# Optimization experiments

Hardware: AMD Instinct MI355X
Metric: run time of the kernel (lower is better)

The kernel has to match this reference:

```python
import jax, jax.numpy as jnp
import numpy as np

NEG_INF = -1.0e9
LEAKY_SLOPE = 0.2


def setup_inputs() -> dict:
    key = jax.random.key(0)
    ks = jax.random.split(key, 8)
    B, H, N, D = 4, 8, 256, 64
    query = jax.random.normal(ks[0], (B, H, N, D), dtype=jnp.float32)
    k_ = jax.random.normal(ks[1], (B, H, N, D), dtype=jnp.float32)
    value = jax.random.normal(ks[2], (B, H, N, D), dtype=jnp.float32)
    mask = jax.random.randint(ks[3], (B, 1, N, N), 0, 2, dtype=jnp.int32)
    # nn.Linear(d_k*2, d_k): weight (D, 2D), bias (D,)
    lim_h = 1.0 / np.sqrt(2 * D)
    W_h = jax.random.uniform(ks[4], (D, 2 * D), minval=-lim_h, maxval=lim_h, dtype=jnp.float32)
    b_h = jax.random.uniform(ks[5], (D,), minval=-lim_h, maxval=lim_h, dtype=jnp.float32)
    # nn.Linear(d_k, 1): weight (1, D), bias (1,)
    lim_o = 1.0 / np.sqrt(D)
    W_o = jax.random.uniform(ks[6], (1, D), minval=-lim_o, maxval=lim_o, dtype=jnp.float32)
    b_o = jax.random.uniform(ks[7], (1,), minval=-lim_o, maxval=lim_o, dtype=jnp.float32)
    return {"query": query, "key": k_, "value": value, "mask": mask,
            "W_h": W_h, "b_h": b_h, "W_o": W_o, "b_o": b_o}


def reference(query, key, value, mask, W_h, b_h, W_o, b_o):
    # W_h acts on concat([q, k]); decompose into two projections (same math):
    # W_h @ [q; k] = q @ W_q^T + k @ W_k^T
    D = query.shape[-1]
    Wq, Wk = W_h[:, :D], W_h[:, D:]
    q_proj = jnp.einsum('bhnd,ed->bhne', query, Wq)  # (B,H,N,D)
    k_proj = jnp.einsum('bhmd,ed->bhme', key, Wk)    # (B,H,N,D)
    # pairwise hidden: (B,H,N,N,D)
    hidden = q_proj[:, :, :, None, :] + k_proj[:, :, None, :, :] + b_h
    hidden = jax.nn.leaky_relu(hidden, negative_slope=LEAKY_SLOPE)
    scores = jnp.einsum('bhnme,e->bhnm', hidden, W_o[0]) + b_o[0]  # (B,H,N,N)
    scores = jnp.where(mask == 0, NEG_INF, scores)
    p_attn = jax.nn.softmax(scores, axis=-1)
    out = jnp.einsum('bhnm,bhmd->bhnd', p_attn, value)
    return out, p_attn
```

## Files before the change

### kernel.cpp

```cpp
#include <hip/hip_runtime.h>

typedef float v2f __attribute__((ext_vector_type(2)));
typedef _Float16 h8 __attribute__((ext_vector_type(8)));

constexpr int B = 4, H = 8, N = 256, D = 64;
constexpr int QBLK = 8;
constexpr int PATTN_OFF = B * H * N * D;
constexpr int NROWS = B * H * N;


__global__ __launch_bounds__(256, 2) void proj_kernel(
    const float* __restrict__ q, const float* __restrict__ k,
    const float* __restrict__ W_h, const float* __restrict__ b_h,
    const float* __restrict__ W_o, const float* __restrict__ b_o,
    float* __restrict__ qp, _Float16* __restrict__ kpbh,
    float* __restrict__ cq6, float* __restrict__ ck6, float* __restrict__ w4)
{
    __shared__ float WT[128 * 65];
    int t = threadIdx.x;
    int lane = t & 63;
    int wid = __builtin_amdgcn_readfirstlane(t >> 6);
    int bid = blockIdx.x;
    int work = (bid & 7) * 64 + (bid >> 3);

    #pragma unroll
    for (int i = 0; i < 8; ++i) {
        int fidx = (t + i * 256) * 4;
        float4 w = *reinterpret_cast<const float4*>(W_h + fidx);
        int e = fidx >> 7, d = fidx & 127;
        WT[(d + 0) * 65 + e] = w.x;
        WT[(d + 1) * 65 + e] = w.y;
        WT[(d + 2) * 65 + e] = w.z;
        WT[(d + 3) * 65 + e] = w.w;
    }
    if (bid == 0 && t < 64) w4[t] = 0.4f * W_o[t];
    __syncthreads();

    int rbase = work * 16 + wid * 4;
    float accq[4] = {}, acck[4] = {};
    #pragma unroll
    for (int d0 = 0; d0 < 64; d0 += 16) {
        float wq[16], wk[16];
        #pragma unroll
        for (int d = 0; d < 16; ++d) {
            wq[d] = WT[(d0 + d) * 65 + lane];
            wk[d] = WT[(64 + d0 + d) * 65 + lane];
        }
        #pragma unroll
        for (int j = 0; j < 4; ++j) {
            const float* qrow = q + (rbase + j) * 64 + d0;
            const float* krow = k + (rbase + j) * 64 + d0;
            #pragma unroll
            for (int d = 0; d < 16; ++d) {
                accq[j] = fmaf(qrow[d], wq[d], accq[j]);
                acck[j] = fmaf(krow[d], wk[d], acck[j]);
            }
        }
    }
    float bh_e = b_h[lane];
    float wo = W_o[lane];
    float bo = b_o[0];
    #pragma unroll
    for (int j = 0; j < 4; ++j) {
        float aq = accq[j];
        float ak = acck[j] + bh_e;
        qp[(rbase + j) * 64 + lane] = aq;
        kpbh[(rbase + j) * 64 + lane] = (_Float16)ak;
        float sq = wo * aq, sk = wo * ak;
        #pragma unroll
        for (int off = 32; off > 0; off >>= 1) {
            sq += __shfl_xor(sq, off, 64);
            sk += __shfl_xor(sk, off, 64);
        }
        if (lane == 0) {
            cq6[rbase + j] = 0.6f * sq + bo;
            ck6[rbase + j] = 0.6f * sk;
        }
    }
}

__global__ __launch_bounds__(512, 2) void attn_kernel(
    const float* __restrict__ qp, const _Float16* __restrict__ kpbh,
    const float* __restrict__ V, const int* __restrict__ mask,
    const float* __restrict__ cq6, const float* __restrict__ ck6,
    const float* __restrict__ w4g,
    float* __restrict__ out)
{
    __shared__ float sc[4096];
    __shared__ _Float16 pf[2048];
    __shared__ float red_s[8][4];

    int t = threadIdx.x;
    int lane = t & 63;
    int wid = __builtin_amdgcn_readfirstlane(t >> 6);
    int h = wid >> 2;
    int m = t & 255;
    int bid = blockIdx.x;
    int work = (bid & 7) * 128 + (bid >> 3);
    int bh = work >> 5;
    int nb = work & 31;
    int b = bh >> 3;
    int n0 = nb * QBLK;
    int kvbase = bh * N * 64;

    const h8* kph = reinterpret_cast<const h8*>(kpbh + kvbase + m * 64 + h * 32);
    h8 kh0 = kph[0], kh1 = kph[1], kh2 = kph[2], kh3 = kph[3];

    float mf[4];
    #pragma unroll
    for (int i = 0; i < 4; ++i)
        mf[i] = (mask[(b * N + n0 + h * 4 + i) * N + m] != 0) ? 1.0f : 0.0f;

    float ckt = (h == 0) ? ck6[bh * N + m] : 0.f;

    v2f sp2[8];
    const float* cq = cq6 + bh * N + n0;
    #pragma unroll
    for (int r = 0; r < 8; ++r) {
        float init = (h == 0) ? (cq[r] + ckt) : 0.f;
        sp2[r] = (v2f){init, 0.f};
    }

    const v2f* qr2 = reinterpret_cast<const v2f*>(qp + (bh * N + n0) * 64 + h * 32);
    const v2f* w42 = reinterpret_cast<const v2f*>(w4g + h * 32);
    #pragma unroll
    for (int chunk = 0; chunk < 4; ++chunk) {
        h8 kc = (chunk == 0) ? kh0 : (chunk == 1) ? kh1 : (chunk == 2) ? kh2 : kh3;
        #pragma unroll
        for (int p = 0; p < 4; ++p) {
            v2f w2 = w42[chunk * 4 + p];
            v2f k2 = (v2f){(float)kc[2 * p], (float)kc[2 * p + 1]};
            #pragma unroll
            for (int r = 0; r < 8; ++r) {
                v2f x = qr2[r * 32 + chunk * 4 + p] + k2;
                v2f ax = __builtin_elementwise_max(x, -x);
                sp2[r] = __builtin_elementwise_fma(w2, ax, sp2[r]);
            }
        }
    }
    #pragma unroll
    for (int r = 0; r < 8; ++r)
        sc[h * 2048 + r * 256 + m] = sp2[r].x + sp2[r].y;

    const float* Vp = V + kvbase + wid * 32 * 64 + lane;
    float vpre[8];
    #pragma unroll
    for (int g = 0; g < 8; ++g) vpre[g] = Vp[g * 64];
    __syncthreads();

    float p8[4];
    #pragma unroll
    for (int i = 0; i < 4; ++i) {
        int rr = h * 4 + i;
        float s = sc[rr * 256 + m] + sc[2048 + rr * 256 + m];
        float p = __expf(s) * mf[i];
        p8[i] = p;
        float l = p;
        #pragma unroll
        for (int off = 32; off > 0; off >>= 1) l += __shfl_xor(l, off, 64);
        if (lane == 0) red_s[wid][i] = l;
    }
    __syncthreads();

    #pragma unroll
    for (int i = 0; i < 4; ++i) {
        int rr = h * 4 + i;
        float gs = red_s[h*4+0][i] + red_s[h*4+1][i] + red_s[h*4+2][i] + red_s[h*4+3][i];
        float pn = p8[i] * __frcp_rn(gs);
        pf[rr * 256 + m] = (_Float16)pn;
        out[PATTN_OFF + (bh * N + n0 + rr) * N + m] = pn;
    }
    __syncthreads();

    float acc[8] = {};
    {
        #pragma unroll
        for (int r = 0; r < 8; ++r) {
            h8 ph = *reinterpret_cast<const h8*>(&pf[r * 256 + wid * 32]);
            #pragma unroll
            for (int g = 0; g < 8; ++g)
                acc[r] = fmaf((float)ph[g], vpre[g], acc[r]);
        }
    }
    #pragma unroll
    for (int j = 8; j < 32; j += 8) {
        float vv[8];
        #pragma unroll
        for (int g = 0; g < 8; ++g) vv[g] = Vp[(j + g) * 64];
        #pragma unroll
        for (int r = 0; r < 8; ++r) {
            h8 ph = *reinterpret_cast<const h8*>(&pf[r * 256 + wid * 32 + j]);
            #pragma unroll
            for (int g = 0; g < 8; ++g)
                acc[r] = fmaf((float)ph[g], vv[g], acc[r]);
        }
    }
    __syncthreads();

    #pragma unroll
    for (int r = 0; r < 8; ++r)
        sc[wid * 512 + r * 64 + lane] = acc[r];
    __syncthreads();

    float o = 0.f;
    #pragma unroll
    for (int mc = 0; mc < 8; ++mc)
        o += sc[mc * 512 + wid * 64 + lane];
    out[(bh * N + n0 + wid) * 64 + lane] = o;
}

extern "C" void kernel_launch(void* const* d_in, const int* in_sizes, int n_in,
                              void* d_out, int out_size, void* d_ws, size_t ws_size,
                              hipStream_t stream) {
    const float* q    = (const float*)d_in[0];
    const float* k    = (const float*)d_in[1];
    const float* v    = (const float*)d_in[2];
    const int*   mask = (const int*)d_in[3];
    const float* W_h  = (const float*)d_in[4];
    const float* b_h  = (const float*)d_in[5];
    const float* W_o  = (const float*)d_in[6];
    const float* b_o  = (const float*)d_in[7];
    float* out = (float*)d_out;

    float* qp       = (float*)d_ws;
    _Float16* kpbh  = (_Float16*)(qp + NROWS * 64);
    float* cq6      = (float*)(qp + NROWS * 64 + NROWS * 64);
    float* ck6      = cq6 + NROWS;
    float* w4       = ck6 + NROWS;

    proj_kernel<<<NROWS / 16, 256, 0, stream>>>(q, k, W_h, b_h, W_o, b_o, qp, kpbh, cq6, ck6, w4);
    attn_kernel<<<B * H * (N / QBLK), 512, 0, stream>>>(qp, kpbh, v, mask, cq6, ck6, w4, out);
}
```

Baseline: 35.12 us.

## Double query rows per attention block and give each wave whole softmax rows

```diff
diff --git a/kernel.cpp b/kernel.cpp
--- a/kernel.cpp
+++ b/kernel.cpp
@@ -4,7 +4,7 @@
 typedef _Float16 h8 __attribute__((ext_vector_type(8)));
 
 constexpr int B = 4, H = 8, N = 256, D = 64;
-constexpr int QBLK = 8;
+constexpr int QBLK = 16;
 constexpr int PATTN_OFF = B * H * N * D;
 constexpr int NROWS = B * H * N;
 
@@ -86,9 +86,8 @@
     const float* __restrict__ w4g,
     float* __restrict__ out)
 {
-    __shared__ float sc[4096];
-    __shared__ _Float16 pf[2048];
-    __shared__ float red_s[8][4];
+    __shared__ float sc[8192];
+    __shared__ _Float16 pf[4096];
 
     int t = threadIdx.x;
     int lane = t & 63;
@@ -96,9 +95,9 @@
     int h = wid >> 2;
     int m = t & 255;
     int bid = blockIdx.x;
-    int work = (bid & 7) * 128 + (bid >> 3);
-    int bh = work >> 5;
-    int nb = work & 31;
+    int work = (bid & 7) * 64 + (bid >> 3);
+    int bh = work >> 4;
+    int nb = work & 15;
     int b = bh >> 3;
     int n0 = nb * QBLK;
     int kvbase = bh * N * 64;
@@ -106,17 +105,21 @@
     const h8* kph = reinterpret_cast<const h8*>(kpbh + kvbase + m * 64 + h * 32);
     h8 kh0 = kph[0], kh1 = kph[1], kh2 = kph[2], kh3 = kph[3];
 
-    float mf[4];
-    #pragma unroll
-    for (int i = 0; i < 4; ++i)
-        mf[i] = (mask[(b * N + n0 + h * 4 + i) * N + m] != 0) ? 1.0f : 0.0f;
+    float mfv[2][4];
+    #pragma unroll
+    for (int j = 0; j < 2; ++j) {
+        int row = n0 + wid + j * 8;
+        #pragma unroll
+        for (int c = 0; c < 4; ++c)
+            mfv[j][c] = (mask[(b * N + row) * N + c * 64 + lane] != 0) ? 1.0f : 0.0f;
+    }
 
     float ckt = (h == 0) ? ck6[bh * N + m] : 0.f;
 
-    v2f sp2[8];
+    v2f sp2[QBLK];
     const float* cq = cq6 + bh * N + n0;
     #pragma unroll
-    for (int r = 0; r < 8; ++r) {
+    for (int r = 0; r < QBLK; ++r) {
         float init = (h == 0) ? (cq[r] + ckt) : 0.f;
         sp2[r] = (v2f){init, 0.f};
     }
@@ -131,7 +134,7 @@
             v2f w2 = w42[chunk * 4 + p];
             v2f k2 = (v2f){(float)kc[2 * p], (float)kc[2 * p + 1]};
             #pragma unroll
-            for (int r = 0; r < 8; ++r) {
+            for (int r = 0; r < QBLK; ++r) {
                 v2f x = qr2[r * 32 + chunk * 4 + p] + k2;
                 v2f ax = __builtin_elementwise_max(x, -x);
                 sp2[r] = __builtin_elementwise_fma(w2, ax, sp2[r]);
@@ -139,8 +142,8 @@
         }
     }
     #pragma unroll
-    for (int r = 0; r < 8; ++r)
-        sc[h * 2048 + r * 256 + m] = sp2[r].x + sp2[r].y;
+    for (int r = 0; r < QBLK; ++r)
+        sc[h * 4096 + r * 256 + m] = sp2[r].x + sp2[r].y;
 
     const float* Vp = V + kvbase + wid * 32 * 64 + lane;
     float vpre[8];
@@ -148,34 +151,36 @@
     for (int g = 0; g < 8; ++g) vpre[g] = Vp[g * 64];
     __syncthreads();
 
-    float p8[4];
-    #pragma unroll
-    for (int i = 0; i < 4; ++i) {
-        int rr = h * 4 + i;
-        float s = sc[rr * 256 + m] + sc[2048 + rr * 256 + m];
-        float p = __expf(s) * mf[i];
-        p8[i] = p;
-        float l = p;
+    #pragma unroll
+    for (int j = 0; j < 2; ++j) {
+        int r = wid + j * 8;
+        float pv4[4];
+        float l = 0.f;
+        #pragma unroll
+        for (int c = 0; c < 4; ++c) {
+            int mm = c * 64 + lane;
+            float s = sc[r * 256 + mm] + sc[4096 + r * 256 + mm];
+            float p = __expf(s) * mfv[j][c];
+            pv4[c] = p;
+            l += p;
+        }
         #pragma unroll
         for (int off = 32; off > 0; off >>= 1) l += __shfl_xor(l, off, 64);
-        if (lane == 0) red_s[wid][i] = l;
-    }
-    __syncthreads();
-
-    #pragma unroll
-    for (int i = 0; i < 4; ++i) {
-        int rr = h * 4 + i;
-        float gs = red_s[h*4+0][i] + red_s[h*4+1][i] + red_s[h*4+2][i] + red_s[h*4+3][i];
-        float pn = p8[i] * __frcp_rn(gs);
-        pf[rr * 256 + m] = (_Float16)pn;
-        out[PATTN_OFF + (bh * N + n0 + rr) * N + m] = pn;
-    }
-    __syncthreads();
-
-    float acc[8] = {};
+        float gs = __frcp_rn(l);
+        #pragma unroll
+        for (int c = 0; c < 4; ++c) {
+            int mm = c * 64 + lane;
+            float pn = pv4[c] * gs;
+            pf[r * 256 + mm] = (_Float16)pn;
+            out[PATTN_OFF + (bh * N + n0 + r) * N + mm] = pn;
+        }
+    }
+    __syncthreads();
+
+    float acc[QBLK] = {};
     {
         #pragma unroll
-        for (int r = 0; r < 8; ++r) {
+        for (int r = 0; r < QBLK; ++r) {
             h8 ph = *reinterpret_cast<const h8*>(&pf[r * 256 + wid * 32]);
             #pragma unroll
             for (int g = 0; g < 8; ++g)
@@ -188,25 +193,27 @@
         #pragma unroll
         for (int g = 0; g < 8; ++g) vv[g] = Vp[(j + g) * 64];
         #pragma unroll
-        for (int r = 0; r < 8; ++r) {
+        for (int r = 0; r < QBLK; ++r) {
             h8 ph = *reinterpret_cast<const h8*>(&pf[r * 256 + wid * 32 + j]);
             #pragma unroll
             for (int g = 0; g < 8; ++g)
                 acc[r] = fmaf((float)ph[g], vv[g], acc[r]);
         }
     }
-    __syncthreads();
-
-    #pragma unroll
-    for (int r = 0; r < 8; ++r)
-        sc[wid * 512 + r * 64 + lane] = acc[r];
-    __syncthreads();
-
-    float o = 0.f;
-    #pragma unroll
-    for (int mc = 0; mc < 8; ++mc)
-        o += sc[mc * 512 + wid * 64 + lane];
-    out[(bh * N + n0 + wid) * 64 + lane] = o;
+    #pragma unroll
+    for (int r = 0; r < QBLK; ++r)
+        sc[wid * 1024 + r * 64 + lane] = acc[r];
+    __syncthreads();
+
+    #pragma unroll
+    for (int j = 0; j < 2; ++j) {
+        int rr = (t >> 6) + j * 8;
+        float o = 0.f;
+        #pragma unroll
+        for (int mc = 0; mc < 8; ++mc)
+            o += sc[mc * 1024 + rr * 64 + lane];
+        out[(bh * N + n0 + rr) * 64 + lane] = o;
+    }
 }
 
 extern "C" void kernel_launch(void* const* d_in, const int* in_sizes, int n_in,
```

Measured after the change: 43.57 us. 1.24x slower.

## Halve attention block to 256 threads, each computing full D score per key

Applied to the files above, without the earlier changes.

```diff
diff --git a/kernel.cpp b/kernel.cpp
--- a/kernel.cpp
+++ b/kernel.cpp
@@ -79,22 +79,21 @@
     }
 }
 
-__global__ __launch_bounds__(512, 2) void attn_kernel(
+__global__ __launch_bounds__(256, 4) void attn_kernel(
     const float* __restrict__ qp, const _Float16* __restrict__ kpbh,
     const float* __restrict__ V, const int* __restrict__ mask,
     const float* __restrict__ cq6, const float* __restrict__ ck6,
     const float* __restrict__ w4g,
     float* __restrict__ out)
 {
-    __shared__ float sc[4096];
     __shared__ _Float16 pf[2048];
-    __shared__ float red_s[8][4];
+    __shared__ float pv[2048];
+    __shared__ float red_s[4][QBLK];
 
     int t = threadIdx.x;
     int lane = t & 63;
     int wid = __builtin_amdgcn_readfirstlane(t >> 6);
-    int h = wid >> 2;
-    int m = t & 255;
+    int m = t;
     int bid = blockIdx.x;
     int work = (bid & 7) * 128 + (bid >> 3);
     int bh = work >> 5;
@@ -103,110 +102,103 @@
     int n0 = nb * QBLK;
     int kvbase = bh * N * 64;
 
-    const h8* kph = reinterpret_cast<const h8*>(kpbh + kvbase + m * 64 + h * 32);
-    h8 kh0 = kph[0], kh1 = kph[1], kh2 = kph[2], kh3 = kph[3];
-
-    float mf[4];
-    #pragma unroll
-    for (int i = 0; i < 4; ++i)
-        mf[i] = (mask[(b * N + n0 + h * 4 + i) * N + m] != 0) ? 1.0f : 0.0f;
-
-    float ckt = (h == 0) ? ck6[bh * N + m] : 0.f;
-
-    v2f sp2[8];
+    const h8* kph = reinterpret_cast<const h8*>(kpbh + kvbase + m * 64);
+    h8 kh[8];
+    #pragma unroll
+    for (int c = 0; c < 8; ++c) kh[c] = kph[c];
+
+    float mf[QBLK];
+    #pragma unroll
+    for (int r = 0; r < QBLK; ++r)
+        mf[r] = (mask[(b * N + n0 + r) * N + m] != 0) ? 1.0f : 0.0f;
+
+    float ckt = ck6[bh * N + m];
+
+    v2f sp2[QBLK];
     const float* cq = cq6 + bh * N + n0;
     #pragma unroll
-    for (int r = 0; r < 8; ++r) {
-        float init = (h == 0) ? (cq[r] + ckt) : 0.f;
-        sp2[r] = (v2f){init, 0.f};
-    }
-
-    const v2f* qr2 = reinterpret_cast<const v2f*>(qp + (bh * N + n0) * 64 + h * 32);
-    const v2f* w42 = reinterpret_cast<const v2f*>(w4g + h * 32);
-    #pragma unroll
-    for (int chunk = 0; chunk < 4; ++chunk) {
-        h8 kc = (chunk == 0) ? kh0 : (chunk == 1) ? kh1 : (chunk == 2) ? kh2 : kh3;
+    for (int r = 0; r < QBLK; ++r) sp2[r] = (v2f){cq[r] + ckt, 0.f};
+
+    const v2f* qr2 = reinterpret_cast<const v2f*>(qp + (bh * N + n0) * 64);
+    const v2f* w42 = reinterpret_cast<const v2f*>(w4g);
+    #pragma unroll
+    for (int c = 0; c < 8; ++c) {
+        h8 kc = kh[c];
         #pragma unroll
         for (int p = 0; p < 4; ++p) {
-            v2f w2 = w42[chunk * 4 + p];
+            v2f w2 = w42[c * 4 + p];
             v2f k2 = (v2f){(float)kc[2 * p], (float)kc[2 * p + 1]};
             #pragma unroll
-            for (int r = 0; r < 8; ++r) {
-                v2f x = qr2[r * 32 + chunk * 4 + p] + k2;
+            for (int r = 0; r < QBLK; ++r) {
+                v2f x = qr2[r * 32 + c * 4 + p] + k2;
                 v2f ax = __builtin_elementwise_max(x, -x);
                 sp2[r] = __builtin_elementwise_fma(w2, ax, sp2[r]);
             }
         }
     }
-    #pragma unroll
-    for (int r = 0; r < 8; ++r)
-        sc[h * 2048 + r * 256 + m] = sp2[r].x + sp2[r].y;
-
-    const float* Vp = V + kvbase + wid * 32 * 64 + lane;
+
+    const float* Vp = V + kvbase + (wid * 64) * 64 + lane;
     float vpre[8];
     #pragma unroll
     for (int g = 0; g < 8; ++g) vpre[g] = Vp[g * 64];
-    __syncthreads();
-
-    float p8[4];
-    #pragma unroll
-    for (int i = 0; i < 4; ++i) {
-        int rr = h * 4 + i;
-        float s = sc[rr * 256 + m] + sc[2048 + rr * 256 + m];
-        float p = __expf(s) * mf[i];
-        p8[i] = p;
+
+    float p8[QBLK];
+    #pragma unroll
+    for (int r = 0; r < QBLK; ++r) {
+        float s = sp2[r].x + sp2[r].y;
+        float p = __expf(s) * mf[r];
+        p8[r] = p;
         float l = p;
         #pragma unroll
         for (int off = 32; off > 0; off >>= 1) l += __shfl_xor(l, off, 64);
-        if (lane == 0) red_s[wid][i] = l;
-    }
-    __syncthreads();
-
-    #pragma unroll
-    for (int i = 0; i < 4; ++i) {
-        int rr = h * 4 + i;
-        float gs = red_s[h*4+0][i] + red_s[h*4+1][i] + red_s[h*4+2][i] + red_s[h*4+3][i];
-        float pn = p8[i] * __frcp_rn(gs);
-        pf[rr * 256 + m] = (_Float16)pn;
-        out[PATTN_OFF + (bh * N + n0 + rr) * N + m] = pn;
-    }
-    __syncthreads();
-
-    float acc[8] = {};
+        if (lane == 0) red_s[wid][r] = l;
+    }
+    __syncthreads();
+
+    #pragma unroll
+    for (int r = 0; r < QBLK; ++r) {
+        float gs = red_s[0][r] + red_s[1][r] + red_s[2][r] + red_s[3][r];
+        float pn = p8[r] * __frcp_rn(gs);
+        pf[r * 256 + m] = (_Float16)pn;
+        out[PATTN_OFF + (bh * N + n0 + r) * N + m] = pn;
+    }
+    __syncthreads();
+
+    float acc[QBLK] = {};
     {
         #pragma unroll
-        for (int r = 0; r < 8; ++r) {
-            h8 ph = *reinterpret_cast<const h8*>(&pf[r * 256 + wid * 32]);
+        for (int r = 0; r < QBLK; ++r) {
+            h8 ph = *reinterpret_cast<const h8*>(&pf[r * 256 + wid * 64]);
             #pragma unroll
             for (int g = 0; g < 8; ++g)
                 acc[r] = fmaf((float)ph[g], vpre[g], acc[r]);
         }
     }
     #pragma unroll
-    for (int j = 8; j < 32; j += 8) {
+    for (int j = 8; j < 64; j += 8) {
         float vv[8];
         #pragma unroll
         for (int g = 0; g < 8; ++g) vv[g] = Vp[(j + g) * 64];
         #pragma unroll
-        for (int r = 0; r < 8; ++r) {
-            h8 ph = *reinterpret_cast<const h8*>(&pf[r * 256 + wid * 32 + j]);
+        for (int r = 0; r < QBLK; ++r) {
+            h8 ph = *reinterpret_cast<const h8*>(&pf[r * 256 + wid * 64 + j]);
             #pragma unroll
             for (int g = 0; g < 8; ++g)
                 acc[r] = fmaf((float)ph[g], vv[g], acc[r]);
         }
     }
-    __syncthreads();
-
-    #pragma unroll
-    for (int r = 0; r < 8; ++r)
-        sc[wid * 512 + r * 64 + lane] = acc[r];
-    __syncthreads();
-
-    float o = 0.f;
-    #pragma unroll
-    for (int mc = 0; mc < 8; ++mc)
-        o += sc[mc * 512 + wid * 64 + lane];
-    out[(bh * N + n0 + wid) * 64 + lane] = o;
+    #pragma unroll
+    for (int r = 0; r < QBLK; ++r)
+        pv[wid * 512 + r * 64 + lane] = acc[r];
+    __syncthreads();
+
+    #pragma unroll
+    for (int j = 0; j < 2; ++j) {
+        int rr = wid + j * 4;
+        float o = pv[0 * 512 + rr * 64 + lane] + pv[1 * 512 + rr * 64 + lane]
+                + pv[2 * 512 + rr * 64 + lane] + pv[3 * 512 + rr * 64 + lane];
+        out[(bh * N + n0 + rr) * 64 + lane] = o;
+    }
 }
 
 extern "C" void kernel_launch(void* const* d_in, const int* in_sizes, int n_in,
@@ -229,5 +221,5 @@
     float* w4       = ck6 + NROWS;
 
     proj_kernel<<<NROWS / 16, 256, 0, stream>>>(q, k, W_h, b_h, W_o, b_o, qp, kpbh, cq6, ck6, w4);
-    attn_kernel<<<B * H * (N / QBLK), 512, 0, stream>>>(qp, kpbh, v, mask, cq6, ck6, w4, out);
+    attn_kernel<<<B * H * (N / QBLK), 256, 0, stream>>>(qp, kpbh, v, mask, cq6, ck6, w4, out);
 }
```

Measured after the change: 42.17 us. +20.1%, slower.
